# Kernel tuning notes

Hardware: AMD Instinct MI355X
Metric: run time of the kernel (lower is better)

## Reference

```python
import jax, jax.numpy as jnp
import numpy as np

N = 33554432
LABEL = 5
PENALIZE_WEIGHT = 3.0
LOWER = LABEL - 0.5
UPPER = LABEL + 0.5


def setup_inputs() -> dict:
    key = jax.random.key(0)
    k1, k2 = jax.random.split(key)
    x = jax.random.normal(k1, (N,), dtype=jnp.float32)
    t = jax.random.randint(k2, (N,), 0, 10, dtype=jnp.int64)
    return {"input": x, "target": t}


def reference(input, target):
    # Fused elementwise mask: weight = penalize_weight where
    # lower < x < upper AND target != label, else 1.0
    x = input
    penal = (x > LOWER) & (x < UPPER) & (target != LABEL)
    w = jnp.where(penal, jnp.float32(PENALIZE_WEIGHT), jnp.float32(1.0))
    diff = x - target.astype(jnp.float32)
    return jnp.mean(w * diff * diff)
```

## Files before the change

### kernel.cpp

```cpp
#include <hip/hip_runtime.h>


#define LABEL_I   5
#define LOWER_F   4.5f
#define UPPER_F   5.5f
#define PENALTY_F 3.0f

typedef float vf4 __attribute__((ext_vector_type(4)));
typedef int   vi4 __attribute__((ext_vector_type(4)));

__device__ __forceinline__ float term(float x, int t) {
    float d = x - (float)t;
    float w = (x > LOWER_F && x < UPPER_F && t != LABEL_I) ? PENALTY_F : 1.0f;
    return w * d * d;
}

__device__ __forceinline__ float term4(vf4 xv, vi4 tv) {
    return term(xv.x, tv.x) + term(xv.y, tv.y) + term(xv.z, tv.z) + term(xv.w, tv.w);
}

#define TPB 1024

__global__ __launch_bounds__(256, 6) void penal_mse_stage1(
        const vf4* __restrict__ x4,
        const vi4* __restrict__ t4,
        float* __restrict__ partials,
        int n4, int tiles, int n_tail_start, int n_total,
        const float* __restrict__ x_scalar,
        const int*  __restrict__ t_scalar) {
    float s0 = 0.0f, s1 = 0.0f, s2 = 0.0f, s3 = 0.0f;

    for (int tile = blockIdx.x; tile < tiles; tile += gridDim.x) {
        int base = tile * TPB + threadIdx.x;
        const vf4* xp = x4 + base;
        const vi4* tp = t4 + base;
        vf4 a0 = __builtin_nontemporal_load(xp);
        vi4 b0 = __builtin_nontemporal_load(tp);
        vf4 a1 = __builtin_nontemporal_load(xp + 256);
        vi4 b1 = __builtin_nontemporal_load(tp + 256);
        vf4 a2 = __builtin_nontemporal_load(xp + 512);
        vi4 b2 = __builtin_nontemporal_load(tp + 512);
        vf4 a3 = __builtin_nontemporal_load(xp + 768);
        vi4 b3 = __builtin_nontemporal_load(tp + 768);
        asm volatile("" : "+v"(a0), "+v"(b0), "+v"(a1), "+v"(b1),
                          "+v"(a2), "+v"(b2), "+v"(a3), "+v"(b3));
        s0 += term4(a0, b0);
        s1 += term4(a1, b1);
        s2 += term4(a2, b2);
        s3 += term4(a3, b3);
    }

    float sum = (s0 + s1) + (s2 + s3);

    for (int i = tiles * TPB + blockIdx.x * blockDim.x + threadIdx.x;
         i < n4; i += gridDim.x * blockDim.x)
        sum += term4(x4[i], t4[i]);

    for (int j = n_tail_start + blockIdx.x * blockDim.x + threadIdx.x;
         j < n_total; j += gridDim.x * blockDim.x)
        sum += term(x_scalar[j], t_scalar[j]);

    #pragma unroll
    for (int off = 32; off > 0; off >>= 1)
        sum += __shfl_down(sum, off, 64);

    __shared__ float wsum[4];
    int lane = threadIdx.x & 63;
    int wave = threadIdx.x >> 6;
    if (lane == 0) wsum[wave] = sum;
    __syncthreads();

    if (threadIdx.x == 0)
        partials[blockIdx.x] = (wsum[0] + wsum[1]) + (wsum[2] + wsum[3]);
}

__global__ __launch_bounds__(256) void penal_mse_stage2(
        const float* __restrict__ partials, int nparts,
        float* __restrict__ out, float inv_n) {
    float sum = 0.0f;
    for (int i = threadIdx.x; i < nparts; i += 256)
        sum += partials[i];

    #pragma unroll
    for (int off = 32; off > 0; off >>= 1)
        sum += __shfl_down(sum, off, 64);

    __shared__ float wsum[4];
    int lane = threadIdx.x & 63;
    int wave = threadIdx.x >> 6;
    if (lane == 0) wsum[wave] = sum;
    __syncthreads();

    if (threadIdx.x == 0)
        out[0] = ((wsum[0] + wsum[1]) + (wsum[2] + wsum[3])) * inv_n;
}

extern "C" void kernel_launch(void* const* d_in, const int* in_sizes, int n_in,
                              void* d_out, int out_size, void* d_ws, size_t ws_size,
                              hipStream_t stream) {
    const float* x = (const float*)d_in[0];
    const int*   t = (const int*)d_in[1];
    float* out = (float*)d_out;
    float* partials = (float*)d_ws;

    int n  = in_sizes[0];
    int n4 = n >> 2;
    int n_tail_start = n4 << 2;
    int tiles = n4 / TPB;
    float inv_n = 1.0f / (float)n;

    const int block = 256;
    const int grid = 2048;

    penal_mse_stage1<<<grid, block, 0, stream>>>(
        (const vf4*)x, (const vi4*)t, partials,
        n4, tiles, n_tail_start, n, x, t);

    penal_mse_stage2<<<1, block, 0, stream>>>(partials, grid, out, inv_n);
}
```

Baseline: 250.0 us.

## Stage loads through LDS with double-buffered global_load_lds and shrink grid

Replaces the direct nontemporal vector loads with `__builtin_amdgcn_global_load_lds` transfers into a per-wave, double-buffered LDS tile. Each iteration prefetches the next tile before consuming the current one. The grid drops from 2048 to 512 blocks so each block runs a longer pipelined loop. The aim is to keep memory requests in flight while computing. Each block now takes 64KB of LDS, which limits occupancy. Also, the `s_waitcnt vmcnt(0)` in the consume step waits on the prefetch just issued, which may remove most of the intended overlap.

```diff
diff --git a/kernel.cpp b/kernel.cpp
--- a/kernel.cpp
+++ b/kernel.cpp
@@ -1,4 +1,5 @@
 #include <hip/hip_runtime.h>
+#include <stdint.h>
 
 
 #define LABEL_I   5
@@ -8,6 +9,10 @@
 
 typedef float vf4 __attribute__((ext_vector_type(4)));
 typedef int   vi4 __attribute__((ext_vector_type(4)));
+
+typedef __attribute__((address_space(1))) const void g_void;
+typedef __attribute__((address_space(3))) void       l_void;
+typedef __attribute__((address_space(3))) char       l_char;
 
 __device__ __forceinline__ float term(float x, int t) {
     float d = x - (float)t;
@@ -19,54 +24,82 @@
     return term(xv.x, tv.x) + term(xv.y, tv.y) + term(xv.z, tv.z) + term(xv.w, tv.w);
 }
 
-#define TPB 1024
+#define TILE_V4 1024
 
-__global__ __launch_bounds__(256, 6) void penal_mse_stage1(
+#define STAGE(buf, tileIdx) do {                                               \
+    int gb = (tileIdx) * TILE_V4 + wave * 256 + lane;                          \
+    const vf4* xp = x4 + gb;                                                   \
+    const vi4* tp = t4 + gb;                                                   \
+    l_char* lx = (l_char*)&ldsx[buf][wave][0];                                 \
+    l_char* lt = (l_char*)&ldst[buf][wave][0];                                 \
+    __builtin_amdgcn_global_load_lds((g_void*)(const void*)(xp),       (l_void*)(lx),        16, 0, 0); \
+    __builtin_amdgcn_global_load_lds((g_void*)(const void*)(tp),       (l_void*)(lt),        16, 0, 0); \
+    __builtin_amdgcn_global_load_lds((g_void*)(const void*)(xp + 64),  (l_void*)(lx + 1024), 16, 0, 0); \
+    __builtin_amdgcn_global_load_lds((g_void*)(const void*)(tp + 64),  (l_void*)(lt + 1024), 16, 0, 0); \
+    __builtin_amdgcn_global_load_lds((g_void*)(const void*)(xp + 128), (l_void*)(lx + 2048), 16, 0, 0); \
+    __builtin_amdgcn_global_load_lds((g_void*)(const void*)(tp + 128), (l_void*)(lt + 2048), 16, 0, 0); \
+    __builtin_amdgcn_global_load_lds((g_void*)(const void*)(xp + 192), (l_void*)(lx + 3072), 16, 0, 0); \
+    __builtin_amdgcn_global_load_lds((g_void*)(const void*)(tp + 192), (l_void*)(lt + 3072), 16, 0, 0); \
+} while (0)
+
+#define CONSUME(buf) do {                                                      \
+    asm volatile("s_waitcnt vmcnt(0) lgkmcnt(0)" ::: "memory");                \
+    const vf4* lxv = (const vf4*)&ldsx[buf][wave][0];                          \
+    const vi4* ltv = (const vi4*)&ldst[buf][wave][0];                          \
+    vf4 X0 = lxv[lane];       vi4 T0 = ltv[lane];                              \
+    vf4 X1 = lxv[lane + 64];  vi4 T1 = ltv[lane + 64];                         \
+    vf4 X2 = lxv[lane + 128]; vi4 T2 = ltv[lane + 128];                        \
+    vf4 X3 = lxv[lane + 192]; vi4 T3 = ltv[lane + 192];                        \
+    s0 += term4(X0, T0); s1 += term4(X1, T1);                                  \
+    s2 += term4(X2, T2); s3 += term4(X3, T3);                                  \
+} while (0)
+
+__global__ __launch_bounds__(256) void penal_mse_stage1(
         const vf4* __restrict__ x4,
         const vi4* __restrict__ t4,
         float* __restrict__ partials,
-        int n4, int tiles, int n_tail_start, int n_total,
+        int n4, int tiles_total, int n_tail_start, int n_total,
         const float* __restrict__ x_scalar,
         const int*  __restrict__ t_scalar) {
+    __shared__ vf4 ldsx[2][4][256];
+    __shared__ vi4 ldst[2][4][256];
+
+    const int wave = threadIdx.x >> 6;
+    const int lane = threadIdx.x & 63;
+
     float s0 = 0.0f, s1 = 0.0f, s2 = 0.0f, s3 = 0.0f;
 
-    for (int tile = blockIdx.x; tile < tiles; tile += gridDim.x) {
-        int base = tile * TPB + threadIdx.x;
-        const vf4* xp = x4 + base;
-        const vi4* tp = t4 + base;
-        vf4 a0 = __builtin_nontemporal_load(xp);
-        vi4 b0 = __builtin_nontemporal_load(tp);
-        vf4 a1 = __builtin_nontemporal_load(xp + 256);
-        vi4 b1 = __builtin_nontemporal_load(tp + 256);
-        vf4 a2 = __builtin_nontemporal_load(xp + 512);
-        vi4 b2 = __builtin_nontemporal_load(tp + 512);
-        vf4 a3 = __builtin_nontemporal_load(xp + 768);
-        vi4 b3 = __builtin_nontemporal_load(tp + 768);
-        asm volatile("" : "+v"(a0), "+v"(b0), "+v"(a1), "+v"(b1),
-                          "+v"(a2), "+v"(b2), "+v"(a3), "+v"(b3));
-        s0 += term4(a0, b0);
-        s1 += term4(a1, b1);
-        s2 += term4(a2, b2);
-        s3 += term4(a3, b3);
+    int ntiles = 0;
+    if ((int)blockIdx.x < tiles_total)
+        ntiles = (tiles_total - 1 - (int)blockIdx.x) / (int)gridDim.x + 1;
+
+    if (ntiles > 0) {
+        STAGE(0, (int)blockIdx.x);
+        int tile = (int)blockIdx.x;
+        for (int i = 0; i < ntiles; ++i) {
+            int buf = i & 1;
+            if (i + 1 < ntiles)
+                STAGE(buf ^ 1, tile + (int)gridDim.x);
+            CONSUME(buf);
+            tile += (int)gridDim.x;
+        }
     }
 
+    for (int i = tiles_total * TILE_V4 + (int)(blockIdx.x * blockDim.x + threadIdx.x);
+         i < n4; i += (int)(gridDim.x * blockDim.x))
+        s0 += term4(x4[i], t4[i]);
+
+    for (int j = n_tail_start + (int)(blockIdx.x * blockDim.x + threadIdx.x);
+         j < n_total; j += (int)(gridDim.x * blockDim.x))
+        s0 += term(x_scalar[j], t_scalar[j]);
+
     float sum = (s0 + s1) + (s2 + s3);
-
-    for (int i = tiles * TPB + blockIdx.x * blockDim.x + threadIdx.x;
-         i < n4; i += gridDim.x * blockDim.x)
-        sum += term4(x4[i], t4[i]);
-
-    for (int j = n_tail_start + blockIdx.x * blockDim.x + threadIdx.x;
-         j < n_total; j += gridDim.x * blockDim.x)
-        sum += term(x_scalar[j], t_scalar[j]);
 
     #pragma unroll
     for (int off = 32; off > 0; off >>= 1)
         sum += __shfl_down(sum, off, 64);
 
     __shared__ float wsum[4];
-    int lane = threadIdx.x & 63;
-    int wave = threadIdx.x >> 6;
     if (lane == 0) wsum[wave] = sum;
     __syncthreads();
 
@@ -106,15 +139,15 @@
     int n  = in_sizes[0];
     int n4 = n >> 2;
     int n_tail_start = n4 << 2;
-    int tiles = n4 / TPB;
+    int tiles_total = n4 / TILE_V4;
     float inv_n = 1.0f / (float)n;
 
     const int block = 256;
-    const int grid = 2048;
+    const int grid = 512;
 
     penal_mse_stage1<<<grid, block, 0, stream>>>(
         (const vf4*)x, (const vi4*)t, partials,
-        n4, tiles, n_tail_start, n, x, t);
+        n4, tiles_total, n_tail_start, n, x, t);
 
     penal_mse_stage2<<<1, block, 0, stream>>>(partials, grid, out, inv_n);
 }
```

Measured after the change: 272.1 us. 8.8% more time.
